# Performance work log

Hardware: AMD Instinct MI355X
Metric: run time of the kernel (lower is better)

The kernel has to match this reference:

```python
import jax, jax.numpy as jnp
import numpy as np

B, T, L = 512, 512, 256
XC, SC, NZ, H, OC = 16, 8, 8, 128, 8
INFO = SC + NZ + 1   # 17: [y, zx, t] channels for the zy (past) encoder
CF = NZ + 1          # 9: [zx, t] channels for the future CDE control
W = 128              # CDEFunc MLP width (width_dfunc default)


def setup_inputs() -> dict:
    key = jax.random.key(0)
    ks = jax.random.split(key, 20)
    rn = lambda k, s: jax.random.normal(k, s, dtype=jnp.float32)
    sc = lambda fan: np.float32(1.0 / np.sqrt(fan))
    return dict(
        y_past=rn(ks[0], (B, L, SC)),
        t=jnp.arange(T, dtype=jnp.float32),
        coeffs_x=rn(ks[1], (B, T, XC)),
        input_length=L,
        zx_wih=rn(ks[2], (3 * H, XC + 1)) * sc(XC + 1),
        zx_whh=rn(ks[3], (3 * H, H)) * sc(H),
        zx_b=rn(ks[4], (3 * H,)) * sc(H),
        zx_bn=rn(ks[5], (H,)) * sc(H),
        zxl_w=rn(ks[6], (NZ, H)) * sc(H),
        zxl_b=rn(ks[7], (NZ,)) * sc(H),
        zy_wih=rn(ks[8], (3 * H, INFO)) * sc(INFO),
        zy_whh=rn(ks[9], (3 * H, H)) * sc(H),
        zy_b=rn(ks[10], (3 * H,)) * sc(H),
        zy_bn=rn(ks[11], (H,)) * sc(H),
        f_w1=rn(ks[12], (W, H)) * sc(H),
        f_b1=rn(ks[13], (W,)) * sc(H),
        f_w2=rn(ks[14], (W, W)) * sc(W),
        f_b2=rn(ks[15], (W,)) * sc(W),
        f_w3=rn(ks[16], (H * CF, W)) * sc(W),
        f_b3=rn(ks[17], (H * CF,)) * sc(W),
        r_w=rn(ks[18], (OC, H)) * sc(H),
        r_b=rn(ks[19], (OC,)) * sc(H),
    )


def _gru(xs, wih, whh, b, bn):
    # xs: (T, B, C). Equinox GRUCell math, batched over B.
    h0 = jnp.zeros((xs.shape[1], whh.shape[1]), xs.dtype)

    def step(h, x):
        i_r, i_z, i_n = jnp.split(x @ wih.T + b, 3, axis=-1)
        g_r, g_z, g_n = jnp.split(h @ whh.T, 3, axis=-1)
        r = jax.nn.sigmoid(i_r + g_r)
        z = jax.nn.sigmoid(i_z + g_z)
        n = jnp.tanh(i_n + r * (g_n + bn))
        hn = n + z * (h - n)  # == new + inp*(hidden-new) in eqx
        return hn, hn

    hT, hs = jax.lax.scan(step, h0, xs)
    return hT, hs


def reference(y_past, t, coeffs_x, input_length,
              zx_wih, zx_whh, zx_b, zx_bn, zxl_w, zxl_b,
              zy_wih, zy_whh, zy_b, zy_bn,
              f_w1, f_b1, f_w2, f_b2, f_w3, f_b3, r_w, r_b):
    Bsz = y_past.shape[0]
    tc = jnp.broadcast_to(t[None, :, None], (Bsz, t.shape[0], 1))
    # --- zx encoder (GRU over control path [X, t]; linear interp at knots == data) ---
    ctrl = jnp.concatenate([coeffs_x, tc], axis=-1)                 # (B,T,XC+1)
    _, hs = _gru(jnp.swapaxes(ctrl, 0, 1), zx_wih, zx_whh, zx_b, zx_bn)
    zx = jnp.swapaxes(hs, 0, 1) @ zxl_w.T + zxl_b                   # (B,T,NZ)
    Lp = input_length
    # --- zy encoder over past control [y, zx, t] (plan_option='full') ---
    ctrl_past = jnp.concatenate([y_past, zx[:, :Lp], tc[:, :Lp]], axis=-1)  # (B,L,INFO)
    zy_current, _ = _gru(jnp.swapaxes(ctrl_past, 0, 1), zy_wih, zy_whh, zy_b, zy_bn)  # (B,H)
    # --- future CDE: dz = f(z) @ dX with linear control X = [zx_future, t_future] ---
    ctrl_fut = jnp.concatenate([zx[:, Lp:], tc[:, Lp:]], axis=-1)   # (B,F,CF)
    dX = jnp.diff(ctrl_fut, axis=1)                                 # (B,F-1,CF)

    def vf(z):  # CDEFunc MLP: (B,H) -> (B,H,CF)
        h1 = jax.nn.softplus(z @ f_w1.T + f_b1)
        h2 = jax.nn.softplus(h1 @ f_w2.T + f_b2)
        o = jnp.tanh(h2 @ f_w3.T + f_b3)
        return o.reshape(z.shape[0], -1, CF)

    def rk4(z, dx):  # one RK4 step per knot interval (dX absorbs dt * slope)
        k1 = jnp.einsum('bhc,bc->bh', vf(z), dx)
        k2 = jnp.einsum('bhc,bc->bh', vf(z + 0.5 * k1), dx)
        k3 = jnp.einsum('bhc,bc->bh', vf(z + 0.5 * k2), dx)
        k4 = jnp.einsum('bhc,bc->bh', vf(z + k3), dx)
        zn = z + (k1 + 2.0 * k2 + 2.0 * k3 + k4) / 6.0
        return zn, zn

    _, zs = jax.lax.scan(rk4, zy_current, jnp.swapaxes(dX, 0, 1))   # (F-1,B,H)
    ys = jnp.concatenate([zy_current[None], zs], axis=0)            # (F,B,H) saveat ts
    y_hat = jnp.swapaxes(ys, 0, 1) @ r_w.T + r_b                    # (B,F,OC)
    return y_hat
```

## Files before the change

kernel.cpp:

```cpp
#include <hip/hip_runtime.h>

#define Bb 512
#define Tt 512
#define Ll 256
#define Ff 256
#define Hh 128
#define H3 384
#define NZ 8
#define XC 16
#define OC 8
#define CF 9
#define W3N 1152
#define BBt 2

__device__ __forceinline__ float sigm(float x){ return 1.0f/(1.0f+expf(-x)); }
__device__ __forceinline__ float softplus_(float x){
  return fmaxf(x, 0.0f) + log1pf(expf(-fabsf(x)));
}
__device__ __forceinline__ float dot4(float4 w, float4 z){
  return w.x*z.x + w.y*z.y + w.z*z.z + w.w*z.w;
}
__device__ __forceinline__ int swz32(int i){ return i ^ ((i >> 3) & 3); }
__device__ __forceinline__ int swzf(int h){ return (((h >> 2) ^ ((h >> 5) & 3)) << 2) + (h & 3); }

__global__ __launch_bounds__(768) void gru_kernel(
    const float* __restrict__ xin, const float* __restrict__ zx_in,
    const float* __restrict__ tin,
    const float* __restrict__ wih, const float* __restrict__ whh,
    const float* __restrict__ bias, const float* __restrict__ bn,
    const float* __restrict__ zxlw, const float* __restrict__ zxlb,
    float* __restrict__ out_zx, float* __restrict__ out_h,
    int steps, int mode)
{
  const int b = blockIdx.x;
  const int tid = threadIdx.x;
  const int j = tid >> 1;
  const int half = tid & 1;

  float wi[17];
  #pragma unroll
  for (int c = 0; c < 17; c++) wi[c] = wih[j*17 + c];
  const float bj = bias[j];
  float4 wr[16];
  {
    const float4* p = reinterpret_cast<const float4*>(whh + (size_t)j*Hh + half*64);
    #pragma unroll
    for (int q = 0; q < 16; q++) wr[q] = p[q];
  }

  __shared__ __align__(16) float s_h[Hh];
  __shared__ float s_i[H3];
  __shared__ float s_g[H3];
  __shared__ float s_x[17];
  __shared__ float s_bn[Hh];
  __shared__ float s_zxlw[NZ*Hh];
  __shared__ float s_red[NZ][17];

  if (tid < Hh){ s_h[tid] = 0.0f; s_bn[tid] = bn[tid]; }
  if (mode == 0){ for (int q = tid; q < NZ*Hh; q += 768) s_zxlw[q] = zxlw[q]; }

  float xreg = 0.f;
  if (tid < 17){
    if (mode == 0){
      xreg = (tid < 16) ? xin[(size_t)b*Tt*XC + tid] : tin[0];
    } else {
      if (tid < 8)       xreg = xin[(size_t)b*Ll*NZ + tid];
      else if (tid < 16) xreg = zx_in[(size_t)b*Tt*NZ + (tid - 8)];
      else               xreg = tin[0];
    }
  }
  __syncthreads();

  for (int t = 0; t < steps; t++){
    if (tid < 17) s_x[tid] = xreg;
    __syncthreads();
    float ai = bj;
    #pragma unroll
    for (int c = 0; c < 17; c++) ai += wi[c]*s_x[c];
    float g0=0.f, g1=0.f, g2=0.f, g3=0.f;
    {
      const float4* h4p = reinterpret_cast<const float4*>(&s_h[half*64]);
      #pragma unroll
      for (int q = 0; q < 16; q++){
        float4 w = wr[q];
        float4 h4 = h4p[q];
        g0 += w.x*h4.x; g1 += w.y*h4.y; g2 += w.z*h4.z; g3 += w.w*h4.w;
      }
    }
    float g = (g0+g1)+(g2+g3);
    g += __shfl_xor(g, 1, 64);
    if (half == 0){ s_i[j] = ai; s_g[j] = g; }
    if (tid < 17 && t + 1 < steps){
      const int tn = t + 1;
      if (mode == 0){
        xreg = (tid < 16) ? xin[(size_t)b*Tt*XC + (size_t)tn*XC + tid] : tin[tn];
      } else {
        if (tid < 8)       xreg = xin[(size_t)b*Ll*NZ + (size_t)tn*NZ + tid];
        else if (tid < 16) xreg = zx_in[(size_t)b*Tt*NZ + (size_t)tn*NZ + (tid - 8)];
        else               xreg = tin[tn];
      }
    }
    __syncthreads();
    if (tid < Hh){
      float r  = sigm(s_i[tid]       + s_g[tid]);
      float zz = sigm(s_i[Hh + tid]  + s_g[Hh + tid]);
      float n  = tanhf(s_i[2*Hh+tid] + r*(s_g[2*Hh+tid] + s_bn[tid]));
      s_h[tid] = n + zz*(s_h[tid] - n);
    }
    __syncthreads();
    if (mode == 0){
      if (tid < Hh){
        int o = tid >> 4, m = tid & 15;
        float p = 0.f;
        #pragma unroll
        for (int q = 0; q < 8; q++) p += s_zxlw[o*Hh + m*8 + q]*s_h[m*8 + q];
        s_red[o][m] = p;
      }
      __syncthreads();
      if (tid < NZ){
        float p = zxlb[tid];
        #pragma unroll
        for (int m = 0; m < 16; m++) p += s_red[tid][m];
        out_zx[(size_t)b*Tt*NZ + (size_t)t*NZ + tid] = p;
      }
      __syncthreads();
    }
  }
  if (mode == 1 && tid < Hh) out_h[b*Hh + tid] = s_h[tid];
}

__global__ __launch_bounds__(512)
__attribute__((amdgpu_waves_per_eu(2, 2)))
void cde_fp32_kernel(
    const float* __restrict__ zy_h, const float* __restrict__ zx,
    const float* __restrict__ tin,
    const float* __restrict__ fw1, const float* __restrict__ fb1,
    const float* __restrict__ fw2, const float* __restrict__ fb2,
    const float* __restrict__ fw3, const float* __restrict__ fb3,
    const float* __restrict__ rw,  const float* __restrict__ rb,
    float* __restrict__ yout)
{
  const int tid = threadIdx.x;
  const int c12 = tid >> 2;
  const int q4  = tid & 3;
  const int col64 = tid >> 3;
  const int e8    = tid & 7;
  const int bg = blockIdx.x * BBt;

  __shared__ __align__(16) float4 s_w1v[4096];
  __shared__ __align__(16) float4 s_w2v[4096];
  __shared__ __align__(16) float4 s_zinv[BBt][32];
  __shared__ __align__(16) float4 s_h1v[BBt][32];
  __shared__ __align__(16) float4 s_h2v[BBt][32];
  __shared__ float s_o[BBt][W3N];
  __shared__ float s_z[BBt][Hh];
  __shared__ float s_kacc[BBt][Hh];
  __shared__ float s_dx[BBt][CF];
  __shared__ float s_rw[OC*Hh];
  __shared__ float s_rb[OC];
  __shared__ float s_b3[W3N];

  float* zin_f0 = reinterpret_cast<float*>(&s_zinv[0][0]);
  float* zin_f1 = reinterpret_cast<float*>(&s_zinv[1][0]);
  float* h1_f0  = reinterpret_cast<float*>(&s_h1v[0][0]);
  float* h1_f1  = reinterpret_cast<float*>(&s_h1v[1][0]);
  float* h2_f0  = reinterpret_cast<float*>(&s_h2v[0][0]);
  float* h2_f1  = reinterpret_cast<float*>(&s_h2v[1][0]);

  for (int idx = tid; idx < Hh*32; idx += 512){
    int col = idx >> 5, jcol = idx & 31;
    int q = jcol >> 3, jj = jcol & 7;
    int dst = jj*512 + col*4 + q;
    s_w1v[dst] = reinterpret_cast<const float4*>(fw1)[idx];
    s_w2v[dst] = reinterpret_cast<const float4*>(fw2)[idx];
  }
  const float b1r = fb1[c12], b2r = fb2[c12];
  for (int idx = tid; idx < W3N; idx += 512) s_b3[idx] = fb3[idx];
  for (int idx = tid; idx < OC*Hh; idx += 512) s_rw[idx] = rw[idx];
  if (tid < OC) s_rb[tid] = rb[tid];
  if (tid < BBt*Hh){
    int b = tid >> 7, h = tid & 127;
    float zv = zy_h[(size_t)(bg + b)*Hh + h];
    s_z[b][h] = zv;
    (b == 0 ? zin_f0 : zin_f1)[swzf(h)] = zv;
  }
  __syncthreads();

  if (tid < 256){
    int b = tid >> 7, r = tid & 127, o = r >> 4, seg = r & 15;
    float p = 0.f;
    #pragma unroll
    for (int q = 0; q < 8; q++)
      p += s_z[b][seg*8 + q]*s_rw[o*Hh + seg*8 + q];
    p += __shfl_xor(p, 1, 64); p += __shfl_xor(p, 2, 64);
    p += __shfl_xor(p, 4, 64); p += __shfl_xor(p, 8, 64);
    if (seg == 0) yout[(size_t)(bg + b)*Ff*OC + o] = s_rb[o] + p;
  }

  const float* w3p = fw3 + (size_t)col64*Hh + e8*16;

  for (int i = 0; i < Ff - 1; i++){
    if (tid < BBt*CF){
      int b = tid/CF, c = tid%CF;
      float d;
      if (c < 8){
        const float* zp = zx + (size_t)(bg + b)*Tt*NZ + (size_t)(Ll + i)*NZ + c;
        d = zp[NZ] - zp[0];
      } else {
        d = tin[Ll + i + 1] - tin[Ll + i];
      }
      s_dx[b][c] = d;
    }
    __syncthreads();

    for (int st = 0; st < 4; st++){
      float4 A0, A1, A2, A3, B0, B1, B2, B3;
      {
        const float4* pA = reinterpret_cast<const float4*>(w3p);
        const float4* pB = reinterpret_cast<const float4*>(w3p + 8192);
        A0 = pA[0]; A1 = pA[1]; A2 = pA[2]; A3 = pA[3];
        B0 = pB[0]; B1 = pB[1]; B2 = pB[2]; B3 = pB[3];
      }
      {
        float p0 = 0.f, p1 = 0.f;
        #pragma unroll
        for (int jj = 0; jj < 8; jj++){
          float4 z0 = s_zinv[0][swz32(q4*8 + jj)];
          float4 z1 = s_zinv[1][swz32(q4*8 + jj)];
          float4 w = s_w1v[jj*512 + tid];
          p0 += dot4(w, z0); p1 += dot4(w, z1);
        }
        p0 += __shfl_xor(p0, 1, 64); p0 += __shfl_xor(p0, 2, 64);
        p1 += __shfl_xor(p1, 1, 64); p1 += __shfl_xor(p1, 2, 64);
        if (q4 == 0){
          h1_f0[swzf(c12)] = softplus_(b1r + p0);
          h1_f1[swzf(c12)] = softplus_(b1r + p1);
        }
      }
      __syncthreads();
      {
        float p0 = 0.f, p1 = 0.f;
        #pragma unroll
        for (int jj = 0; jj < 8; jj++){
          float4 z0 = s_h1v[0][swz32(q4*8 + jj)];
          float4 z1 = s_h1v[1][swz32(q4*8 + jj)];
          float4 w = s_w2v[jj*512 + tid];
          p0 += dot4(w, z0); p1 += dot4(w, z1);
        }
        p0 += __shfl_xor(p0, 1, 64); p0 += __shfl_xor(p0, 2, 64);
        p1 += __shfl_xor(p1, 1, 64); p1 += __shfl_xor(p1, 2, 64);
        if (q4 == 0){
          h2_f0[swzf(c12)] = softplus_(b2r + p0);
          h2_f1[swzf(c12)] = softplus_(b2r + p1);
        }
      }
      __syncthreads();
      {
        float4 h2a0 = s_h2v[0][swz32(e8*4 + 0)];
        float4 h2a1 = s_h2v[0][swz32(e8*4 + 1)];
        float4 h2a2 = s_h2v[0][swz32(e8*4 + 2)];
        float4 h2a3 = s_h2v[0][swz32(e8*4 + 3)];
        float4 h2b0 = s_h2v[1][swz32(e8*4 + 0)];
        float4 h2b1 = s_h2v[1][swz32(e8*4 + 1)];
        float4 h2b2 = s_h2v[1][swz32(e8*4 + 2)];
        float4 h2b3 = s_h2v[1][swz32(e8*4 + 3)];
        #pragma unroll 2
        for (int g = 0; g < 18; g++){
          float4 c0, c1, c2, c3;
          if ((g & 1) == 0){
            c0 = A0; c1 = A1; c2 = A2; c3 = A3;
            if (g + 2 < 18){
              const float4* pF = reinterpret_cast<const float4*>(w3p + (size_t)(g+2)*8192);
              A0 = pF[0]; A1 = pF[1]; A2 = pF[2]; A3 = pF[3];
            }
          } else {
            c0 = B0; c1 = B1; c2 = B2; c3 = B3;
            if (g + 2 < 18){
              const float4* pF = reinterpret_cast<const float4*>(w3p + (size_t)(g+2)*8192);
              B0 = pF[0]; B1 = pF[1]; B2 = pF[2]; B3 = pF[3];
            }
          }
          float p0 = dot4(c0, h2a0) + dot4(c1, h2a1) + dot4(c2, h2a2) + dot4(c3, h2a3);
          float p1 = dot4(c0, h2b0) + dot4(c1, h2b1) + dot4(c2, h2b2) + dot4(c3, h2b3);
          p0 += __shfl_xor(p0, 1, 64); p0 += __shfl_xor(p0, 2, 64); p0 += __shfl_xor(p0, 4, 64);
          p1 += __shfl_xor(p1, 1, 64); p1 += __shfl_xor(p1, 2, 64); p1 += __shfl_xor(p1, 4, 64);
          if (e8 == 0){
            int n = g*64 + col64;
            s_o[0][n] = s_b3[n] + p0;
            s_o[1][n] = s_b3[n] + p1;
          }
        }
      }
      __syncthreads();
      if (tid < BBt*Hh){
        int b = tid >> 7, h = tid & 127;
        float kc = 0.f;
        #pragma unroll
        for (int c = 0; c < CF; c++)
          kc += tanhf(s_o[b][h*CF + c]) * s_dx[b][c];
        float zv = s_z[b][h], zin;
        if      (st == 0){ s_kacc[b][h] = kc;        zin = zv + 0.5f*kc; }
        else if (st == 1){ s_kacc[b][h] += 2.f*kc;   zin = zv + 0.5f*kc; }
        else if (st == 2){ s_kacc[b][h] += 2.f*kc;   zin = zv + kc; }
        else { float zn = zv + (s_kacc[b][h] + kc)*(1.f/6.f); s_z[b][h] = zn; zin = zn; }
        (b == 0 ? zin_f0 : zin_f1)[swzf(h)] = zin;
      }
      __syncthreads();
    }
    if (tid < 256){
      int b = tid >> 7, r = tid & 127, o = r >> 4, seg = r & 15;
      float p = 0.f;
      #pragma unroll
      for (int q = 0; q < 8; q++)
        p += s_z[b][seg*8 + q]*s_rw[o*Hh + seg*8 + q];
      p += __shfl_xor(p, 1, 64); p += __shfl_xor(p, 2, 64);
      p += __shfl_xor(p, 4, 64); p += __shfl_xor(p, 8, 64);
      if (seg == 0) yout[(size_t)(bg + b)*Ff*OC + (size_t)(i + 1)*OC + o] = s_rb[o] + p;
    }
  }
}

extern "C" void kernel_launch(void* const* d_in, const int* in_sizes, int n_in,
                              void* d_out, int out_size, void* d_ws, size_t ws_size,
                              hipStream_t stream)
{
  (void)in_sizes; (void)n_in; (void)out_size; (void)ws_size;
  const float* y_past = (const float*)d_in[0];
  const float* t_in   = (const float*)d_in[1];
  const float* coeffs = (const float*)d_in[2];
  const float* zx_wih = (const float*)d_in[4];
  const float* zx_whh = (const float*)d_in[5];
  const float* zx_b   = (const float*)d_in[6];
  const float* zx_bn  = (const float*)d_in[7];
  const float* zxl_w  = (const float*)d_in[8];
  const float* zxl_b  = (const float*)d_in[9];
  const float* zy_wih = (const float*)d_in[10];
  const float* zy_whh = (const float*)d_in[11];
  const float* zy_b   = (const float*)d_in[12];
  const float* zy_bn  = (const float*)d_in[13];
  const float* fw1 = (const float*)d_in[14];
  const float* fb1 = (const float*)d_in[15];
  const float* fw2 = (const float*)d_in[16];
  const float* fb2 = (const float*)d_in[17];
  const float* fw3 = (const float*)d_in[18];
  const float* fb3 = (const float*)d_in[19];
  const float* r_w = (const float*)d_in[20];
  const float* r_b = (const float*)d_in[21];

  float* ws = (float*)d_ws;
  float* zx_buf = ws;
  float* zy_buf = ws + (size_t)Bb*Tt*NZ;

  gru_kernel<<<Bb, 768, 0, stream>>>(coeffs, nullptr, t_in,
                                     zx_wih, zx_whh, zx_b, zx_bn,
                                     zxl_w, zxl_b, zx_buf, nullptr, Tt, 0);
  gru_kernel<<<Bb, 768, 0, stream>>>(y_past, zx_buf, t_in,
                                     zy_wih, zy_whh, zy_b, zy_bn,
                                     nullptr, nullptr, nullptr, zy_buf, Ll, 1);
  cde_fp32_kernel<<<Bb/BBt, 512, 0, stream>>>(zy_buf, zx_buf, t_in,
                                              fw1, fb1, fw2, fb2, fw3, fb3,
                                              r_w, r_b, (float*)d_out);
}
```

Measured before the change: 14.47 ms.

## Double CDE block to 1024 threads with 8-lane splits and DPP reductions

Result: slower. 25.92 ms (+79.1%).

```diff
diff --git a/kernel.cpp b/kernel.cpp
--- a/kernel.cpp
+++ b/kernel.cpp
@@ -22,6 +22,16 @@
 }
 __device__ __forceinline__ int swz32(int i){ return i ^ ((i >> 3) & 3); }
 __device__ __forceinline__ int swzf(int h){ return (((h >> 2) ^ ((h >> 5) & 3)) << 2) + (h & 3); }
+__device__ __forceinline__ float red8(float p){
+  int t;
+  t = __builtin_amdgcn_mov_dpp(__builtin_bit_cast(int, p), 0xB1, 0xF, 0xF, true);
+  p += __builtin_bit_cast(float, t);
+  t = __builtin_amdgcn_mov_dpp(__builtin_bit_cast(int, p), 0x4E, 0xF, 0xF, true);
+  p += __builtin_bit_cast(float, t);
+  t = __builtin_amdgcn_ds_swizzle(__builtin_bit_cast(int, p), 0x101F);
+  p += __builtin_bit_cast(float, t);
+  return p;
+}
 
 __global__ __launch_bounds__(768) void gru_kernel(
     const float* __restrict__ xin, const float* __restrict__ zx_in,
@@ -129,8 +139,8 @@
   if (mode == 1 && tid < Hh) out_h[b*Hh + tid] = s_h[tid];
 }
 
-__global__ __launch_bounds__(512)
-__attribute__((amdgpu_waves_per_eu(2, 2)))
+__global__ __launch_bounds__(1024)
+__attribute__((amdgpu_waves_per_eu(4, 4)))
 void cde_fp32_kernel(
     const float* __restrict__ zy_h, const float* __restrict__ zx,
     const float* __restrict__ tin,
@@ -141,10 +151,8 @@
     float* __restrict__ yout)
 {
   const int tid = threadIdx.x;
-  const int c12 = tid >> 2;
-  const int q4  = tid & 3;
-  const int col64 = tid >> 3;
-  const int e8    = tid & 7;
+  const int colG = tid >> 3;
+  const int e8   = tid & 7;
   const int bg = blockIdx.x * BBt;
 
   __shared__ __align__(16) float4 s_w1v[4096];
@@ -167,16 +175,16 @@
   float* h2_f0  = reinterpret_cast<float*>(&s_h2v[0][0]);
   float* h2_f1  = reinterpret_cast<float*>(&s_h2v[1][0]);
 
-  for (int idx = tid; idx < Hh*32; idx += 512){
-    int col = idx >> 5, jcol = idx & 31;
-    int q = jcol >> 3, jj = jcol & 7;
-    int dst = jj*512 + col*4 + q;
+  for (int idx = tid; idx < Hh*32; idx += 1024){
+    int col = idx >> 5, rem = idx & 31;
+    int e = rem >> 2, r = rem & 3;
+    int dst = r*1024 + col*8 + e;
     s_w1v[dst] = reinterpret_cast<const float4*>(fw1)[idx];
     s_w2v[dst] = reinterpret_cast<const float4*>(fw2)[idx];
   }
-  const float b1r = fb1[c12], b2r = fb2[c12];
-  for (int idx = tid; idx < W3N; idx += 512) s_b3[idx] = fb3[idx];
-  for (int idx = tid; idx < OC*Hh; idx += 512) s_rw[idx] = rw[idx];
+  const float b1r = fb1[colG], b2r = fb2[colG];
+  for (int idx = tid; idx < W3N; idx += 1024) s_b3[idx] = fb3[idx];
+  s_rw[tid] = rw[tid];
   if (tid < OC) s_rb[tid] = rb[tid];
   if (tid < BBt*Hh){
     int b = tid >> 7, h = tid & 127;
@@ -197,7 +205,7 @@
     if (seg == 0) yout[(size_t)(bg + b)*Ff*OC + o] = s_rb[o] + p;
   }
 
-  const float* w3p = fw3 + (size_t)col64*Hh + e8*16;
+  const float* w3p = fw3 + (size_t)colG*Hh + e8*16;
 
   for (int i = 0; i < Ff - 1; i++){
     if (tid < BBt*CF){
@@ -217,41 +225,39 @@
       float4 A0, A1, A2, A3, B0, B1, B2, B3;
       {
         const float4* pA = reinterpret_cast<const float4*>(w3p);
-        const float4* pB = reinterpret_cast<const float4*>(w3p + 8192);
+        const float4* pB = reinterpret_cast<const float4*>(w3p + 16384);
         A0 = pA[0]; A1 = pA[1]; A2 = pA[2]; A3 = pA[3];
         B0 = pB[0]; B1 = pB[1]; B2 = pB[2]; B3 = pB[3];
       }
       {
         float p0 = 0.f, p1 = 0.f;
         #pragma unroll
-        for (int jj = 0; jj < 8; jj++){
-          float4 z0 = s_zinv[0][swz32(q4*8 + jj)];
-          float4 z1 = s_zinv[1][swz32(q4*8 + jj)];
-          float4 w = s_w1v[jj*512 + tid];
+        for (int r = 0; r < 4; r++){
+          float4 z0 = s_zinv[0][swz32(e8*4 + r)];
+          float4 z1 = s_zinv[1][swz32(e8*4 + r)];
+          float4 w = s_w1v[r*1024 + tid];
           p0 += dot4(w, z0); p1 += dot4(w, z1);
         }
-        p0 += __shfl_xor(p0, 1, 64); p0 += __shfl_xor(p0, 2, 64);
-        p1 += __shfl_xor(p1, 1, 64); p1 += __shfl_xor(p1, 2, 64);
-        if (q4 == 0){
-          h1_f0[swzf(c12)] = softplus_(b1r + p0);
-          h1_f1[swzf(c12)] = softplus_(b1r + p1);
+        p0 = red8(p0); p1 = red8(p1);
+        if (e8 == 0){
+          h1_f0[swzf(colG)] = softplus_(b1r + p0);
+          h1_f1[swzf(colG)] = softplus_(b1r + p1);
         }
       }
       __syncthreads();
       {
         float p0 = 0.f, p1 = 0.f;
         #pragma unroll
-        for (int jj = 0; jj < 8; jj++){
-          float4 z0 = s_h1v[0][swz32(q4*8 + jj)];
-          float4 z1 = s_h1v[1][swz32(q4*8 + jj)];
-          float4 w = s_w2v[jj*512 + tid];
+        for (int r = 0; r < 4; r++){
+          float4 z0 = s_h1v[0][swz32(e8*4 + r)];
+          float4 z1 = s_h1v[1][swz32(e8*4 + r)];
+          float4 w = s_w2v[r*1024 + tid];
           p0 += dot4(w, z0); p1 += dot4(w, z1);
         }
-        p0 += __shfl_xor(p0, 1, 64); p0 += __shfl_xor(p0, 2, 64);
-        p1 += __shfl_xor(p1, 1, 64); p1 += __shfl_xor(p1, 2, 64);
-        if (q4 == 0){
-          h2_f0[swzf(c12)] = softplus_(b2r + p0);
-          h2_f1[swzf(c12)] = softplus_(b2r + p1);
+        p0 = red8(p0); p1 = red8(p1);
+        if (e8 == 0){
+          h2_f0[swzf(colG)] = softplus_(b2r + p0);
+          h2_f1[swzf(colG)] = softplus_(b2r + p1);
         }
       }
       __syncthreads();
@@ -265,27 +271,26 @@
         float4 h2b2 = s_h2v[1][swz32(e8*4 + 2)];
         float4 h2b3 = s_h2v[1][swz32(e8*4 + 3)];
         #pragma unroll 2
-        for (int g = 0; g < 18; g++){
+        for (int g = 0; g < 9; g++){
           float4 c0, c1, c2, c3;
           if ((g & 1) == 0){
             c0 = A0; c1 = A1; c2 = A2; c3 = A3;
-            if (g + 2 < 18){
-              const float4* pF = reinterpret_cast<const float4*>(w3p + (size_t)(g+2)*8192);
+            if (g + 2 < 9){
+              const float4* pF = reinterpret_cast<const float4*>(w3p + (size_t)(g+2)*16384);
               A0 = pF[0]; A1 = pF[1]; A2 = pF[2]; A3 = pF[3];
             }
           } else {
             c0 = B0; c1 = B1; c2 = B2; c3 = B3;
-            if (g + 2 < 18){
-              const float4* pF = reinterpret_cast<const float4*>(w3p + (size_t)(g+2)*8192);
+            if (g + 2 < 9){
+              const float4* pF = reinterpret_cast<const float4*>(w3p + (size_t)(g+2)*16384);
               B0 = pF[0]; B1 = pF[1]; B2 = pF[2]; B3 = pF[3];
             }
           }
           float p0 = dot4(c0, h2a0) + dot4(c1, h2a1) + dot4(c2, h2a2) + dot4(c3, h2a3);
           float p1 = dot4(c0, h2b0) + dot4(c1, h2b1) + dot4(c2, h2b2) + dot4(c3, h2b3);
-          p0 += __shfl_xor(p0, 1, 64); p0 += __shfl_xor(p0, 2, 64); p0 += __shfl_xor(p0, 4, 64);
-          p1 += __shfl_xor(p1, 1, 64); p1 += __shfl_xor(p1, 2, 64); p1 += __shfl_xor(p1, 4, 64);
+          p0 = red8(p0); p1 = red8(p1);
           if (e8 == 0){
-            int n = g*64 + col64;
+            int n = g*128 + colG;
             s_o[0][n] = s_b3[n] + p0;
             s_o[1][n] = s_b3[n] + p1;
           }
@@ -357,7 +362,7 @@
   gru_kernel<<<Bb, 768, 0, stream>>>(y_past, zx_buf, t_in,
                                      zy_wih, zy_whh, zy_b, zy_bn,
                                      nullptr, nullptr, nullptr, zy_buf, Ll, 1);
-  cde_fp32_kernel<<<Bb/BBt, 512, 0, stream>>>(zy_buf, zx_buf, t_in,
-                                              fw1, fb1, fw2, fb2, fw3, fb3,
-                                              r_w, r_b, (float*)d_out);
-}
+  cde_fp32_kernel<<<Bb/BBt, 1024, 0, stream>>>(zy_buf, zx_buf, t_in,
+                                               fw1, fb1, fw2, fb2, fw3, fb3,
+                                               r_w, r_b, (float*)d_out);
+}
```
